# Kernel tuning notes

Hardware: AMD Instinct MI355X
Metric: run time of the kernel (lower is better)

## Reference

```python
import jax, jax.numpy as jnp
import numpy as np

N_LOC = 20000
N_EXP = 200000
H = 64
E = 1500000
L = 400000


def setup_inputs() -> dict:
    key = jax.random.key(0)
    ks = jax.random.split(key, 24)
    f = jnp.float32
    w = lambda k, shp: jax.random.normal(k, shp, dtype=f) * 0.1
    # edges: ('location','of','experts'): src in [0,N_LOC), dst in [0,N_EXP)
    src = jax.random.randint(ks[0], (E,), 0, N_LOC)
    dst = jax.random.randint(ks[1], (E,), 0, N_EXP)
    edge_of = jnp.stack([src, dst])          # location -> experts
    edge_rev = jnp.stack([dst, src])         # experts -> location (ToUndirected)
    row = jax.random.randint(ks[2], (L,), 0, N_LOC)
    col = jax.random.randint(ks[3], (L,), 0, N_EXP)
    edge_label_index = jnp.stack([row, col])
    return dict(
        emb_loc=w(ks[4], (N_LOC, H)), emb_exp=w(ks[5], (N_EXP, H)),
        W1l_of=w(ks[6], (H, H)), b1_of=jnp.zeros((H,), f), W1r_of=w(ks[7], (H, H)),
        W1l_rev=w(ks[8], (H, H)), b1_rev=jnp.zeros((H,), f), W1r_rev=w(ks[9], (H, H)),
        W2l_of=w(ks[10], (H, H)), b2_of=jnp.zeros((H,), f), W2r_of=w(ks[11], (H, H)),
        W2l_rev=w(ks[12], (H, H)), b2_rev=jnp.zeros((H,), f), W2r_rev=w(ks[13], (H, H)),
        dW1=w(ks[14], (2 * H, H)), db1=jnp.zeros((H,), f),
        dW2=w(ks[15], (H, 1)), db2=jnp.zeros((1,), f),
        edge_of=edge_of, edge_rev=edge_rev, edge_label_index=edge_label_index,
    )


def _sage(x_src, x_dst, edge, Wl, b, Wr, n_dst):
    # PyG SAGEConv: lin_l(mean of neighbor msgs) + lin_r(x_dst); bias only in lin_l
    s, d = edge[0], edge[1]
    msg = x_src[s]                                   # [E, H] gather
    summed = jax.ops.segment_sum(msg, d, num_segments=n_dst)
    cnt = jax.ops.segment_sum(jnp.ones((edge.shape[1],), x_src.dtype), d, num_segments=n_dst)
    agg = summed / jnp.maximum(cnt, 1.0)[:, None]
    return agg @ Wl + b + x_dst @ Wr


def reference(emb_loc, emb_exp,
              W1l_of, b1_of, W1r_of, W1l_rev, b1_rev, W1r_rev,
              W2l_of, b2_of, W2r_of, W2l_rev, b2_rev, W2r_rev,
              dW1, db1, dW2, db2,
              edge_of, edge_rev, edge_label_index):
    # layer 1 (to_hetero: one conv per edge type; each dst type has one incoming type)
    z_exp = jax.nn.relu(_sage(emb_loc, emb_exp, edge_of, W1l_of, b1_of, W1r_of, N_EXP))
    z_loc = jax.nn.relu(_sage(emb_exp, emb_loc, edge_rev, W1l_rev, b1_rev, W1r_rev, N_LOC))
    # layer 2 (no relu)
    z_exp2 = _sage(z_loc, z_exp, edge_of, W2l_of, b2_of, W2r_of, N_EXP)
    z_loc2 = _sage(z_exp, z_loc, edge_rev, W2l_rev, b2_rev, W2r_rev, N_LOC)
    # EdgeDecoder: gather-concat-MLP
    row, col = edge_label_index[0], edge_label_index[1]
    z = jnp.concatenate([z_loc2[row], z_exp2[col]], axis=-1)  # [L, 2H]
    h = jax.nn.relu(z @ dW1 + db1)
    out = (h @ dW2 + db2).reshape(-1)
    return out
```

## Files before the change

### kernel.cpp

```cpp
#include <hip/hip_runtime.h>

#define H 64
#define NE 1500000
#define NLOC 20000
#define NEXP 200000
#define NL 400000
#define PAD_E 32
#define PAD_L 128

#define EB 896
#define NBE 224
#define LB 112
#define NBL 179
#define BIN_CHUNK 2048
#define NBIN ((NE + BIN_CHUNK - 1) / BIN_CHUNK)
#define EBSLOT 28
#define LBSLOT 32
#define ECAP 8192
#define LCAP 10240
#define FCAP 4096

#define WS_NEED 90546112ULL

typedef int vint4 __attribute__((ext_vector_type(4)));
typedef _Float16 f16x8 __attribute__((ext_vector_type(8)));
typedef float f32x4 __attribute__((ext_vector_type(4)));
typedef unsigned int u32;
typedef unsigned short u16;
typedef unsigned long long u64;

__device__ __forceinline__ float bcastf(float v, int k) {
  return __int_as_float(__builtin_amdgcn_readlane(__float_as_int(v), k));
}
__device__ __forceinline__ int bcasti(int v, int k) {
  return __builtin_amdgcn_readlane(v, k);
}

__global__ __launch_bounds__(256) void bin_kernel(
    const int* __restrict__ src, const int* __restrict__ dst,
    u32* __restrict__ expQ, u32* __restrict__ locQ,
    int* __restrict__ qcnt, int* __restrict__ flbk_cnt,
    u64* __restrict__ flbkQ)
{
  __shared__ u32 eb[NBE * EBSLOT];
  __shared__ u32 lb[NBL * LBSLOT];
  __shared__ int ec[NBE], lc[NBL], ebase[NBE], lbase[NBL];

  const int tid = threadIdx.x;
  for (int i = tid; i < NBE; i += 256) ec[i] = 0;
  for (int i = tid; i < NBL; i += 256) lc[i] = 0;
  __syncthreads();

  const long base = (long)blockIdx.x * BIN_CHUNK + tid * 8;
  if (base < NE) {
    vint4 s0 = __builtin_nontemporal_load((const vint4*)(src + base));
    vint4 s1 = __builtin_nontemporal_load((const vint4*)(src + base + 4));
    vint4 d0 = __builtin_nontemporal_load((const vint4*)(dst + base));
    vint4 d1 = __builtin_nontemporal_load((const vint4*)(dst + base + 4));
    int ss[8] = {s0.x, s0.y, s0.z, s0.w, s1.x, s1.y, s1.z, s1.w};
    int dd[8] = {d0.x, d0.y, d0.z, d0.w, d1.x, d1.y, d1.z, d1.w};
#pragma unroll
    for (int k = 0; k < 8; k++) {
      const u32 d = (u32)dd[k], s = (u32)ss[k];
      {
        const u32 b = d / (u32)EB;
        const int pos = atomicAdd(&ec[b], 1);
        if (pos < EBSLOT) {
          eb[b * EBSLOT + pos] = ((d - b * EB) << 16) | s;
        } else {
          int fi = atomicAdd(flbk_cnt, 1);
          if (fi < FCAP) flbkQ[fi] = ((u64)d << 32) | (u64)s;
        }
      }
      {
        const u32 b = s / (u32)LB;
        const int pos = atomicAdd(&lc[b], 1);
        if (pos < LBSLOT) {
          lb[b * LBSLOT + pos] = ((s - b * LB) << 18) | d;
        } else {
          int fi = atomicAdd(flbk_cnt, 1);
          if (fi < FCAP) flbkQ[fi] = (1ULL << 63) | ((u64)s << 32) | (u64)d;
        }
      }
    }
  }
  __syncthreads();

  for (int i = tid; i < NBE; i += 256) {
    const int c = min(ec[i], EBSLOT);
    ebase[i] = c ? atomicAdd(&qcnt[i], c) : 0;
  }
  for (int i = tid; i < NBL; i += 256) {
    const int c = min(lc[i], LBSLOT);
    lbase[i] = c ? atomicAdd(&qcnt[NBE + i], c) : 0;
  }
  __syncthreads();

  const int wid = tid >> 6, ln = tid & 63;
  for (int b = wid; b < NBE; b += 4) {
    const int c = min(ec[b], EBSLOT);
    if (ln < c) {
      const int idx = ebase[b] + ln;
      const u32 r = eb[b * EBSLOT + ln];
      if (idx < ECAP) {
        expQ[(long)b * ECAP + idx] = r;
      } else {
        int fi = atomicAdd(flbk_cnt, 1);
        if (fi < FCAP)
          flbkQ[fi] = ((u64)(b * EB + (r >> 16)) << 32) | (u64)(r & 0xFFFF);
      }
    }
  }
  for (int b = wid; b < NBL; b += 4) {
    const int c = min(lc[b], LBSLOT);
    if (ln < c) {
      const int idx = lbase[b] + ln;
      const u32 r = lb[b * LBSLOT + ln];
      if (idx < LCAP) {
        locQ[(long)b * LCAP + idx] = r;
      } else {
        int fi = atomicAdd(flbk_cnt, 1);
        if (fi < FCAP)
          flbkQ[fi] = (1ULL << 63) | ((u64)(b * LB + (r >> 18)) << 32) |
                      (u64)(r & 0x3FFFF);
      }
    }
  }
}

__global__ __launch_bounds__(256) void build_kernel(
    const u32* __restrict__ expQ, const u32* __restrict__ locQ,
    const int* __restrict__ qcnt,
    u16* __restrict__ nbr_exp, int* __restrict__ nbr_loc,
    int* __restrict__ cnt_exp, int* __restrict__ cnt_loc)
{
  __shared__ char ldsraw[60928];
  const int tid = threadIdx.x;
  if (blockIdx.x < NBE) {
    const int b = blockIdx.x;
    u16* rows = (u16*)ldsraw;
    int* cnts = (int*)(ldsraw + 57344);
    for (int i = tid; i < EB; i += 256) cnts[i] = 0;
    __syncthreads();
    const int n = min(qcnt[b], ECAP);
    for (int i = tid; i < n; i += 256) {
      const u32 r = expQ[(long)b * ECAP + i];
      const int nl = (int)(r >> 16);
      const int pos = atomicAdd(&cnts[nl], 1);
      if (pos < PAD_E) rows[nl * PAD_E + pos] = (u16)(r & 0xFFFF);
    }
    __syncthreads();
    const int node0 = b * EB;
    const int nn = min(EB, NEXP - node0);
    u32* grows = (u32*)(nbr_exp + (long)node0 * PAD_E);
    const u32* lrows = (const u32*)rows;
    for (int j = tid; j < nn * (PAD_E / 2); j += 256) grows[j] = lrows[j];
    for (int i = tid; i < nn; i += 256) cnt_exp[node0 + i] = cnts[i];
  } else {
    const int b = blockIdx.x - NBE;
    int* rows = (int*)ldsraw;
    int* cnts = (int*)(ldsraw + 57344);
    for (int i = tid; i < LB; i += 256) cnts[i] = 0;
    __syncthreads();
    const int n = min(qcnt[NBE + b], LCAP);
    for (int i = tid; i < n; i += 256) {
      const u32 r = locQ[(long)b * LCAP + i];
      const int sl = (int)(r >> 18);
      const int pos = atomicAdd(&cnts[sl], 1);
      if (pos < PAD_L) rows[sl * PAD_L + pos] = (int)(r & 0x3FFFF);
    }
    __syncthreads();
    const int node0 = b * LB;
    const int nn = min(LB, NLOC - node0);
    int* grows = nbr_loc + (long)node0 * PAD_L;
    for (int j = tid; j < nn * PAD_L; j += 256) grows[j] = rows[j];
    for (int i = tid; i < nn; i += 256) cnt_loc[node0 + i] = cnts[i];
  }
}

__global__ __launch_bounds__(256) void fold_kernel(
    const float* __restrict__ W2r_of, const float* __restrict__ W2l_of,
    const float* __restrict__ W2l_rev, const float* __restrict__ W2r_rev,
    const float* __restrict__ dW1, const float* __restrict__ b2_of,
    const float* __restrict__ b2_rev,
    float* __restrict__ Wf_q, float* __restrict__ Wf_y2,
    float* __restrict__ Wf_t2, float* __restrict__ Wf_p,
    float* __restrict__ bf_q, float* __restrict__ bf_p,
    const int* __restrict__ flbk_cnt, const u64* __restrict__ flbkQ,
    u16* __restrict__ nbr_exp, int* __restrict__ nbr_loc,
    int* __restrict__ cnt_exp, int* __restrict__ cnt_loc)
{
  const int lane = threadIdx.x & 63;
  const int w = threadIdx.x >> 6;
  const float* dW1a = dW1;
  const float* dW1b = dW1 + H * H;
  if (blockIdx.x < 4) {
    const float* A; const float* B; float* C;
    switch (blockIdx.x) {
      case 0:  A = W2r_of;  B = dW1b; C = Wf_q;  break;
      case 1:  A = W2l_of;  B = dW1b; C = Wf_y2; break;
      case 2:  A = W2l_rev; B = dW1a; C = Wf_t2; break;
      default: A = W2r_rev; B = dW1a; C = Wf_p;  break;
    }
    float b[H];
#pragma unroll
    for (int k = 0; k < H; k++) b[k] = B[k * H + lane];
    for (int r = w * 16; r < w * 16 + 16; r++) {
      const float xv = A[r * H + lane];
      float a0 = 0.f, a1 = 0.f;
#pragma unroll
      for (int k = 0; k < H; k += 2) {
        a0 += bcastf(xv, k)     * b[k];
        a1 += bcastf(xv, k + 1) * b[k + 1];
      }
      C[r * H + lane] = a0 + a1;
    }
  } else if (blockIdx.x == 4) {
    if (w < 2) {
      const float* bv_src = (w == 0) ? b2_of : b2_rev;
      const float* B      = (w == 0) ? dW1b  : dW1a;
      float* o            = (w == 0) ? bf_q  : bf_p;
      float wk[H];
#pragma unroll
      for (int k = 0; k < H; k++) wk[k] = B[k * H + lane];
      const float bv = bv_src[lane];
      float a = 0.f;
#pragma unroll
      for (int k = 0; k < H; k++) a += bcastf(bv, k) * wk[k];
      o[lane] = a;
    }
  } else {
    const int n = min(*flbk_cnt, FCAP);
    for (int i = threadIdx.x; i < n; i += 256) {
      const u64 rec = flbkQ[i];
      const int node = (int)((rec >> 32) & 0x3FFFF);
      const int val  = (int)(rec & 0x3FFFF);
      if ((rec >> 63) == 0) {
        int pos = atomicAdd(&cnt_exp[node], 1);
        if (pos < PAD_E) nbr_exp[(long)node * PAD_E + pos] = (u16)val;
      } else {
        int pos = atomicAdd(&cnt_loc[node], 1);
        if (pos < PAD_L) nbr_loc[(long)node * PAD_L + pos] = val;
      }
    }
  }
}

__global__ __launch_bounds__(256, 4) void dense_linear_kernel(
    const float* __restrict__ x, _Float16* __restrict__ out16,
    const float* __restrict__ W, int n)
{
  const int lane = threadIdx.x & 63;
  const int gw = (blockIdx.x * 256 + threadIdx.x) >> 6;
  const int nw = (gridDim.x * 256) >> 6;
  float w[H];
#pragma unroll
  for (int k = 0; k < H; k++) w[k] = W[k * H + lane];
  for (int i = gw; i < n; i += nw) {
    const float xv = x[i * H + lane];
    float a0 = 0.f, a1 = 0.f;
#pragma unroll
    for (int k = 0; k < H; k += 2) {
      a0 += bcastf(xv, k)     * w[k];
      a1 += bcastf(xv, k + 1) * w[k + 1];
    }
    out16[i * H + lane] = (_Float16)(a0 + a1);
  }
}

__global__ __launch_bounds__(256, 4) void mfma_pass_kernel(
    const unsigned short* __restrict__ nbr, const int* __restrict__ cnt,
    const _Float16* __restrict__ y,
    const float* a32, const _Float16* a16,
    _Float16* out1, const float* __restrict__ W1,
    const float* __restrict__ bias, int relu,
    _Float16* out2, const float* __restrict__ W2)
{
  const int w = threadIdx.x >> 6;
  const int lane = threadIdx.x & 63;
  const int q = lane >> 4;
  const int cidx = lane & 15;
  const int rb = blockIdx.x * 16;

  __shared__ float Gs[16 * H];

  f16x8 b1lo, b1hi, b2lo, b2hi;
#pragma unroll
  for (int j = 0; j < 8; j++) {
    b1lo[j] = (_Float16)W1[(q * 8 + j) * H + w * 16 + cidx];
    b1hi[j] = (_Float16)W1[(32 + q * 8 + j) * H + w * 16 + cidx];
  }
  if (out2) {
#pragma unroll
    for (int j = 0; j < 8; j++) {
      b2lo[j] = (_Float16)W2[(q * 8 + j) * H + w * 16 + cidx];
      b2hi[j] = (_Float16)W2[(32 + q * 8 + j) * H + w * 16 + cidx];
    }
  }

  if (y) {
    for (int rr = 0; rr < 4; rr++) {
      const int i = rb + w * 4 + rr;
      const int c = cnt[i];
      const int cc = min(c, PAD_E);
      const unsigned short* nb = nbr + (long)i * PAD_E;
      float s0 = 0.f, s1 = 0.f, s2 = 0.f, s3 = 0.f;
      const int id = (lane < cc) ? (int)nb[lane] : 0;
      int k = 0;
      const int m4 = cc & ~3;
      for (; k < m4; k += 4) {
        const int i0 = bcasti(id, k), i1 = bcasti(id, k + 1),
                  i2 = bcasti(id, k + 2), i3 = bcasti(id, k + 3);
        s0 += (float)y[(long)i0 * H + lane];
        s1 += (float)y[(long)i1 * H + lane];
        s2 += (float)y[(long)i2 * H + lane];
        s3 += (float)y[(long)i3 * H + lane];
      }
      for (; k < cc; k++) s0 += (float)y[(long)bcasti(id, k) * H + lane];
      Gs[(w * 4 + rr) * H + lane] =
          ((s0 + s1) + (s2 + s3)) / fmaxf((float)c, 1.0f);
    }
  }

  f16x8 a0, a1;
  if (a16) {
    const _Float16* ar = a16 + (long)(rb + cidx) * H;
    a0 = *(const f16x8*)(ar + q * 8);
    a1 = *(const f16x8*)(ar + 32 + q * 8);
  } else {
    const float* ar = a32 + (long)(rb + cidx) * H;
#pragma unroll
    for (int j = 0; j < 8; j++) {
      a0[j] = (_Float16)ar[q * 8 + j];
      a1[j] = (_Float16)ar[32 + q * 8 + j];
    }
  }
  f32x4 acc1 = {0.f, 0.f, 0.f, 0.f};
  acc1 = __builtin_amdgcn_mfma_f32_16x16x32_f16(a0, b1lo, acc1, 0, 0, 0);
  acc1 = __builtin_amdgcn_mfma_f32_16x16x32_f16(a1, b1hi, acc1, 0, 0, 0);
  f32x4 acc2 = {0.f, 0.f, 0.f, 0.f};
  if (out2) {
    acc2 = __builtin_amdgcn_mfma_f32_16x16x32_f16(a0, b2lo, acc2, 0, 0, 0);
    acc2 = __builtin_amdgcn_mfma_f32_16x16x32_f16(a1, b2hi, acc2, 0, 0, 0);
  }

  const float bj = bias ? bias[w * 16 + cidx] : 0.f;
  __syncthreads();
#pragma unroll
  for (int reg = 0; reg < 4; reg++) {
    const int r = q * 4 + reg;
    float v = acc1[reg] + bj;
    if (y) v += Gs[r * H + w * 16 + cidx];
    if (relu) v = fmaxf(v, 0.f);
    out1[(long)(rb + r) * H + w * 16 + cidx] = (_Float16)v;
    if (out2)
      out2[(long)(rb + r) * H + w * 16 + cidx] = (_Float16)acc2[reg];
  }
}

__global__ __launch_bounds__(256, 4) void loc_gather_kernel(
    const int* __restrict__ nbr, const int* __restrict__ cnt,
    const _Float16* __restrict__ T, const float* __restrict__ x,
    float* __restrict__ out32, _Float16* __restrict__ out16,
    const float* __restrict__ Wr, const float* __restrict__ bias,
    int n, int relu)
{
  const int lane = threadIdx.x & 63;
  const int gw = (blockIdx.x * 256 + threadIdx.x) >> 6;
  const int nw = (gridDim.x * 256) >> 6;
  float wr[H];
#pragma unroll
  for (int k = 0; k < H; k++) wr[k] = Wr[k * H + lane];
  const float bj = bias[lane];
  for (int i = gw; i < n; i += nw) {
    const int c = cnt[i];
    const int cc = min(c, PAD_L);
    const int* nb = nbr + (long)i * PAD_L;
    float s0 = 0.f, s1 = 0.f, s2 = 0.f, s3 = 0.f;
    int e = 0;
    while (e < cc) {
      const int m = min(cc - e, 64);
      const int id = (lane < m) ? nb[e + lane] : 0;
      int k = 0;
      const int m4 = m & ~3;
      for (; k < m4; k += 4) {
        const int i0 = bcasti(id, k), i1 = bcasti(id, k + 1),
                  i2 = bcasti(id, k + 2), i3 = bcasti(id, k + 3);
        s0 += (float)T[(long)i0 * H + lane];
        s1 += (float)T[(long)i1 * H + lane];
        s2 += (float)T[(long)i2 * H + lane];
        s3 += (float)T[(long)i3 * H + lane];
      }
      for (; k < m; k++) s0 += (float)T[(long)bcasti(id, k) * H + lane];
      e += m;
    }
    const float agg = ((s0 + s1) + (s2 + s3)) / fmaxf((float)c, 1.0f);
    const float xv = x[i * H + lane];
    float a0 = 0.f, a1 = 0.f;
#pragma unroll
    for (int k = 0; k < H; k += 2) {
      a0 += bcastf(xv, k)     * wr[k];
      a1 += bcastf(xv, k + 1) * wr[k + 1];
    }
    float acc = agg + bj + a0 + a1;
    if (relu) acc = fmaxf(acc, 0.0f);
    if (out32) out32[i * H + lane] = acc;
    else       out16[i * H + lane] = (_Float16)acc;
  }
}

__global__ __launch_bounds__(256, 4) void edge_kernel(
    const int* __restrict__ row, const int* __restrict__ col,
    const _Float16* __restrict__ P, const _Float16* __restrict__ Q,
    const float* __restrict__ db1, const float* __restrict__ dW2,
    const float* __restrict__ db2, float* __restrict__ out)
{
  const int lane = threadIdx.x & 63;
  const int gw = (blockIdx.x * 256 + threadIdx.x) >> 6;
  const int nw = (gridDim.x * 256) >> 6;
  const float bj = db1[lane];
  const float w2 = dW2[lane];
  const float b2 = db2[0];
  for (int e = gw * 4; e < NL; e += nw * 4) {
    const int n4 = min(NL - e, 4);
    float h[4];
#pragma unroll
    for (int k = 0; k < 4; k++) {
      if (k < n4) {
        const int r = row[e + k], c = col[e + k];
        const float p = (float)P[(long)r * H + lane];
        const float q = (float)Q[(long)c * H + lane];
        h[k] = fmaxf(p + q + bj, 0.0f) * w2;
      } else h[k] = 0.f;
    }
#pragma unroll
    for (int off = 1; off < 64; off <<= 1) {
#pragma unroll
      for (int k = 0; k < 4; k++) h[k] += __shfl_xor(h[k], off);
    }
    if (lane == 0) {
#pragma unroll
      for (int k = 0; k < 4; k++)
        if (k < n4) out[e + k] = h[k] + b2;
    }
  }
}

extern "C" void kernel_launch(void* const* d_in, const int* in_sizes, int n_in,
                              void* d_out, int out_size, void* d_ws, size_t ws_size,
                              hipStream_t stream) {
  const float* emb_loc = (const float*)d_in[0];
  const float* emb_exp = (const float*)d_in[1];
  const float* W1l_of  = (const float*)d_in[2];
  const float* b1_of   = (const float*)d_in[3];
  const float* W1r_of  = (const float*)d_in[4];
  const float* W1l_rev = (const float*)d_in[5];
  const float* b1_rev  = (const float*)d_in[6];
  const float* W1r_rev = (const float*)d_in[7];
  const float* W2l_of  = (const float*)d_in[8];
  const float* b2_of   = (const float*)d_in[9];
  const float* W2r_of  = (const float*)d_in[10];
  const float* W2l_rev = (const float*)d_in[11];
  const float* b2_rev  = (const float*)d_in[12];
  const float* W2r_rev = (const float*)d_in[13];
  const float* dW1     = (const float*)d_in[14];
  const float* db1     = (const float*)d_in[15];
  const float* dW2     = (const float*)d_in[16];
  const float* db2     = (const float*)d_in[17];
  const int*   edge_of = (const int*)d_in[18];
  const int*   eli     = (const int*)d_in[20];

  const int* src = edge_of;
  const int* dst = edge_of + NE;
  const int* row = eli;
  const int* col = eli + NL;

  if (ws_size < WS_NEED) return;

  char* ws = (char*)d_ws;
  int*            cnt_loc = (int*)(ws);
  int*            cnt_exp = (int*)(ws + 80000);
  int*            nbr_loc = (int*)(ws + 880064);
  unsigned short* nbr_exp = (unsigned short*)(ws + 11120064);
  _Float16*       Ylh     = (_Float16*)(ws + 23920064);
  _Float16*       Y2fh    = (_Float16*)(ws + 26480064);
  float*          z_loc   = (float*)(ws + 29040064);
  _Float16*       PH      = (_Float16*)(ws + 34160064);
  _Float16*       ZE      = (_Float16*)(ws + 39280064);
  _Float16*       TH      = (_Float16*)(ws + 64880064);
  u32*            expQ    = (u32*)(ws + 64880064);
  u32*            locQ    = (u32*)(ws + 72220096);
  int*            qcnt    = (int*)(ws + 79551936);
  int*            flbk    = (int*)(ws + 79553552);
  u64*            flbkQ   = (u64*)(ws + 79554048);
  float*          Wf_q    = (float*)(ws + 90480064);
  float*          Wf_y2   = (float*)(ws + 90496448);
  float*          Wf_t2   = (float*)(ws + 90512832);
  float*          Wf_p    = (float*)(ws + 90529216);
  float*          bf_q    = (float*)(ws + 90545600);
  float*          bf_p    = (float*)(ws + 90545856);
  float*          out     = (float*)d_out;

  (void)hipMemsetAsync(ws + 79551936, 0, 2048, stream);

  bin_kernel<<<NBIN, 256, 0, stream>>>(src, dst, expQ, locQ, qcnt, flbk, flbkQ);
  build_kernel<<<NBE + NBL, 256, 0, stream>>>(expQ, locQ, qcnt,
      nbr_exp, nbr_loc, cnt_exp, cnt_loc);
  fold_kernel<<<6, 256, 0, stream>>>(W2r_of, W2l_of, W2l_rev, W2r_rev,
                                     dW1, b2_of, b2_rev,
                                     Wf_q, Wf_y2, Wf_t2, Wf_p, bf_q, bf_p,
                                     flbk, flbkQ, nbr_exp, nbr_loc,
                                     cnt_exp, cnt_loc);

  dense_linear_kernel<<<1280, 256, 0, stream>>>(emb_loc, Ylh, W1l_of, NLOC);
  mfma_pass_kernel<<<NEXP / 16, 256, 0, stream>>>(nbr_exp, cnt_exp, Ylh,
      emb_exp, (const _Float16*)nullptr, ZE, W1r_of, b1_of, 1, TH, W1l_rev);
  loc_gather_kernel<<<1250, 256, 0, stream>>>(nbr_loc, cnt_loc, TH,
      emb_loc, z_loc, (_Float16*)nullptr, W1r_rev, b1_rev, NLOC, 1);

  dense_linear_kernel<<<1280, 256, 0, stream>>>(z_loc, Y2fh, Wf_y2, NLOC);
  mfma_pass_kernel<<<NEXP / 16, 256, 0, stream>>>(nbr_exp, cnt_exp, Y2fh,
      (const float*)nullptr, ZE, ZE, Wf_q, bf_q, 0, TH, Wf_t2);
  loc_gather_kernel<<<1250, 256, 0, stream>>>(nbr_loc, cnt_loc, TH,
      z_loc, (float*)nullptr, PH, Wf_p, bf_p, NLOC, 0);

  edge_kernel<<<2048, 256, 0, stream>>>(row, col, PH, ZE,
                                        db1, dW2, db2, out);
}
```

Measured before the change: 527.1 us.

## Fuse first dense linear into prep kernel and interleave neighbor gathers for ILP

Merges the layer-1 location dense linear (emb_loc @ W1l_of) into the weight-folding prep kernel, which saves one launch. In mfma_pass the A-operand loads are vectorized and moved ahead of the neighbor gather. The gather now loops over four rows at once so more independent loads are in flight, and the shared buffer is padded to 68 floats per row. loc_gather now handles two nodes per wave with interleaved gathers. The cost is more branchy predicated loops, and the dense linear now runs on only 314 blocks instead of 1280.

```diff
diff --git a/kernel.cpp b/kernel.cpp
--- a/kernel.cpp
+++ b/kernel.cpp
@@ -178,7 +178,7 @@
   }
 }
 
-__global__ __launch_bounds__(256) void fold_kernel(
+__global__ __launch_bounds__(256) void prep_kernel(
     const float* __restrict__ W2r_of, const float* __restrict__ W2l_of,
     const float* __restrict__ W2l_rev, const float* __restrict__ W2r_rev,
     const float* __restrict__ dW1, const float* __restrict__ b2_of,
@@ -188,7 +188,9 @@
     float* __restrict__ bf_q, float* __restrict__ bf_p,
     const int* __restrict__ flbk_cnt, const u64* __restrict__ flbkQ,
     u16* __restrict__ nbr_exp, int* __restrict__ nbr_loc,
-    int* __restrict__ cnt_exp, int* __restrict__ cnt_loc)
+    int* __restrict__ cnt_exp, int* __restrict__ cnt_loc,
+    const float* __restrict__ emb_loc, _Float16* __restrict__ Ylh,
+    const float* __restrict__ W1l_of)
 {
   const int lane = threadIdx.x & 63;
   const int w = threadIdx.x >> 6;
@@ -229,7 +231,7 @@
       for (int k = 0; k < H; k++) a += bcastf(bv, k) * wk[k];
       o[lane] = a;
     }
-  } else {
+  } else if (blockIdx.x == 5) {
     const int n = min(*flbk_cnt, FCAP);
     for (int i = threadIdx.x; i < n; i += 256) {
       const u64 rec = flbkQ[i];
@@ -243,6 +245,23 @@
         if (pos < PAD_L) nbr_loc[(long)node * PAD_L + pos] = val;
       }
     }
+  } else {
+    float wreg[H];
+#pragma unroll
+    for (int k = 0; k < H; k++) wreg[k] = W1l_of[k * H + lane];
+    const int rbase = (blockIdx.x - 6) * 64 + w * 16;
+    for (int rr = 0; rr < 16; rr++) {
+      const int r = rbase + rr;
+      if (r >= NLOC) break;
+      const float xv = emb_loc[(long)r * H + lane];
+      float a0 = 0.f, a1 = 0.f;
+#pragma unroll
+      for (int k = 0; k < H; k += 2) {
+        a0 += bcastf(xv, k)     * wreg[k];
+        a1 += bcastf(xv, k + 1) * wreg[k + 1];
+      }
+      Ylh[(long)r * H + lane] = (_Float16)(a0 + a1);
+    }
   }
 }
 
@@ -269,7 +288,7 @@
 }
 
 __global__ __launch_bounds__(256, 4) void mfma_pass_kernel(
-    const unsigned short* __restrict__ nbr, const int* __restrict__ cnt,
+    const u16* __restrict__ nbr, const int* __restrict__ cnt,
     const _Float16* __restrict__ y,
     const float* a32, const _Float16* a16,
     _Float16* out1, const float* __restrict__ W1,
@@ -282,7 +301,7 @@
   const int cidx = lane & 15;
   const int rb = blockIdx.x * 16;
 
-  __shared__ float Gs[16 * H];
+  __shared__ float Gs[16 * 68];
 
   f16x8 b1lo, b1hi, b2lo, b2hi;
 #pragma unroll
@@ -295,30 +314,6 @@
     for (int j = 0; j < 8; j++) {
       b2lo[j] = (_Float16)W2[(q * 8 + j) * H + w * 16 + cidx];
       b2hi[j] = (_Float16)W2[(32 + q * 8 + j) * H + w * 16 + cidx];
-    }
-  }
-
-  if (y) {
-    for (int rr = 0; rr < 4; rr++) {
-      const int i = rb + w * 4 + rr;
-      const int c = cnt[i];
-      const int cc = min(c, PAD_E);
-      const unsigned short* nb = nbr + (long)i * PAD_E;
-      float s0 = 0.f, s1 = 0.f, s2 = 0.f, s3 = 0.f;
-      const int id = (lane < cc) ? (int)nb[lane] : 0;
-      int k = 0;
-      const int m4 = cc & ~3;
-      for (; k < m4; k += 4) {
-        const int i0 = bcasti(id, k), i1 = bcasti(id, k + 1),
-                  i2 = bcasti(id, k + 2), i3 = bcasti(id, k + 3);
-        s0 += (float)y[(long)i0 * H + lane];
-        s1 += (float)y[(long)i1 * H + lane];
-        s2 += (float)y[(long)i2 * H + lane];
-        s3 += (float)y[(long)i3 * H + lane];
-      }
-      for (; k < cc; k++) s0 += (float)y[(long)bcasti(id, k) * H + lane];
-      Gs[(w * 4 + rr) * H + lane] =
-          ((s0 + s1) + (s2 + s3)) / fmaxf((float)c, 1.0f);
     }
   }
 
@@ -329,12 +324,48 @@
     a1 = *(const f16x8*)(ar + 32 + q * 8);
   } else {
     const float* ar = a32 + (long)(rb + cidx) * H;
-#pragma unroll
-    for (int j = 0; j < 8; j++) {
-      a0[j] = (_Float16)ar[q * 8 + j];
-      a1[j] = (_Float16)ar[32 + q * 8 + j];
-    }
-  }
+    f32x4 v0 = *(const f32x4*)(ar + q * 8);
+    f32x4 v1 = *(const f32x4*)(ar + q * 8 + 4);
+    f32x4 v2 = *(const f32x4*)(ar + 32 + q * 8);
+    f32x4 v3 = *(const f32x4*)(ar + 32 + q * 8 + 4);
+#pragma unroll
+    for (int j = 0; j < 4; j++) {
+      a0[j] = (_Float16)v0[j];
+      a0[j + 4] = (_Float16)v1[j];
+      a1[j] = (_Float16)v2[j];
+      a1[j + 4] = (_Float16)v3[j];
+    }
+  }
+
+  if (y) {
+    const int i0r = rb + w * 4;
+    int c4[4];
+#pragma unroll
+    for (int rr = 0; rr < 4; rr++) c4[rr] = cnt[i0r + rr];
+    int id4[4];
+#pragma unroll
+    for (int rr = 0; rr < 4; rr++) {
+      const int c = min(c4[rr], PAD_E);
+      id4[rr] = (lane < c) ? (int)nbr[(long)(i0r + rr) * PAD_E + lane] : 0;
+    }
+    float sa[4] = {0.f, 0.f, 0.f, 0.f}, sb[4] = {0.f, 0.f, 0.f, 0.f};
+    const int cm = min(max(max(c4[0], c4[1]), max(c4[2], c4[3])), PAD_E);
+    for (int k = 0; k < cm; k += 2) {
+#pragma unroll
+      for (int rr = 0; rr < 4; rr++) {
+        const int c = min(c4[rr], PAD_E);
+        if (k < c)
+          sa[rr] += (float)y[(long)bcasti(id4[rr], k) * H + lane];
+        if (k + 1 < c)
+          sb[rr] += (float)y[(long)bcasti(id4[rr], k + 1) * H + lane];
+      }
+    }
+#pragma unroll
+    for (int rr = 0; rr < 4; rr++)
+      Gs[(w * 4 + rr) * 68 + lane] =
+          (sa[rr] + sb[rr]) / fmaxf((float)c4[rr], 1.0f);
+  }
+
   f32x4 acc1 = {0.f, 0.f, 0.f, 0.f};
   acc1 = __builtin_amdgcn_mfma_f32_16x16x32_f16(a0, b1lo, acc1, 0, 0, 0);
   acc1 = __builtin_amdgcn_mfma_f32_16x16x32_f16(a1, b1hi, acc1, 0, 0, 0);
@@ -350,7 +381,7 @@
   for (int reg = 0; reg < 4; reg++) {
     const int r = q * 4 + reg;
     float v = acc1[reg] + bj;
-    if (y) v += Gs[r * H + w * 16 + cidx];
+    if (y) v += Gs[r * 68 + w * 16 + cidx];
     if (relu) v = fmaxf(v, 0.f);
     out1[(long)(rb + r) * H + w * 16 + cidx] = (_Float16)v;
     if (out2)
@@ -372,40 +403,52 @@
 #pragma unroll
   for (int k = 0; k < H; k++) wr[k] = Wr[k * H + lane];
   const float bj = bias[lane];
-  for (int i = gw; i < n; i += nw) {
-    const int c = cnt[i];
-    const int cc = min(c, PAD_L);
-    const int* nb = nbr + (long)i * PAD_L;
-    float s0 = 0.f, s1 = 0.f, s2 = 0.f, s3 = 0.f;
-    int e = 0;
-    while (e < cc) {
-      const int m = min(cc - e, 64);
-      const int id = (lane < m) ? nb[e + lane] : 0;
-      int k = 0;
-      const int m4 = m & ~3;
-      for (; k < m4; k += 4) {
-        const int i0 = bcasti(id, k), i1 = bcasti(id, k + 1),
-                  i2 = bcasti(id, k + 2), i3 = bcasti(id, k + 3);
-        s0 += (float)T[(long)i0 * H + lane];
-        s1 += (float)T[(long)i1 * H + lane];
-        s2 += (float)T[(long)i2 * H + lane];
-        s3 += (float)T[(long)i3 * H + lane];
-      }
-      for (; k < m; k++) s0 += (float)T[(long)bcasti(id, k) * H + lane];
-      e += m;
-    }
-    const float agg = ((s0 + s1) + (s2 + s3)) / fmaxf((float)c, 1.0f);
-    const float xv = x[i * H + lane];
-    float a0 = 0.f, a1 = 0.f;
+  for (int i = gw * 2; i < n; i += nw * 2) {
+    const int c0 = cnt[i], c1 = cnt[i + 1];
+    const int cc0 = min(c0, PAD_L), cc1 = min(c1, PAD_L);
+    const int* nb0 = nbr + (long)i * PAD_L;
+    const int* nb1 = nb0 + PAD_L;
+    float s0a = 0.f, s0b = 0.f, s1a = 0.f, s1b = 0.f;
+    for (int e = 0; e < PAD_L; e += 64) {
+      const int m0 = min(cc0 - e, 64);
+      const int m1 = min(cc1 - e, 64);
+      if (m0 <= 0 && m1 <= 0) break;
+      const int id0 = (lane < m0) ? nb0[e + lane] : 0;
+      const int id1 = (lane < m1) ? nb1[e + lane] : 0;
+      const int km = max(m0, m1);
+      for (int k = 0; k < km; k += 2) {
+        if (k < m0)
+          s0a += (float)T[(long)bcasti(id0, k) * H + lane];
+        if (k + 1 < m0)
+          s0b += (float)T[(long)bcasti(id0, k + 1) * H + lane];
+        if (k < m1)
+          s1a += (float)T[(long)bcasti(id1, k) * H + lane];
+        if (k + 1 < m1)
+          s1b += (float)T[(long)bcasti(id1, k + 1) * H + lane];
+      }
+    }
+    const float agg0 = (s0a + s0b) / fmaxf((float)c0, 1.0f);
+    const float agg1 = (s1a + s1b) / fmaxf((float)c1, 1.0f);
+    const float xv0 = x[(long)i * H + lane];
+    const float xv1 = x[(long)(i + 1) * H + lane];
+    float a00 = 0.f, a01 = 0.f, a10 = 0.f, a11 = 0.f;
 #pragma unroll
     for (int k = 0; k < H; k += 2) {
-      a0 += bcastf(xv, k)     * wr[k];
-      a1 += bcastf(xv, k + 1) * wr[k + 1];
-    }
-    float acc = agg + bj + a0 + a1;
-    if (relu) acc = fmaxf(acc, 0.0f);
-    if (out32) out32[i * H + lane] = acc;
-    else       out16[i * H + lane] = (_Float16)acc;
+      a00 += bcastf(xv0, k)     * wr[k];
+      a01 += bcastf(xv0, k + 1) * wr[k + 1];
+      a10 += bcastf(xv1, k)     * wr[k];
+      a11 += bcastf(xv1, k + 1) * wr[k + 1];
+    }
+    float acc0 = agg0 + bj + a00 + a01;
+    float acc1 = agg1 + bj + a10 + a11;
+    if (relu) { acc0 = fmaxf(acc0, 0.0f); acc1 = fmaxf(acc1, 0.0f); }
+    if (out32) {
+      out32[(long)i * H + lane] = acc0;
+      out32[(long)(i + 1) * H + lane] = acc1;
+    } else {
+      out16[(long)i * H + lane] = (_Float16)acc0;
+      out16[(long)(i + 1) * H + lane] = (_Float16)acc1;
+    }
   }
 }
 
@@ -506,13 +549,13 @@
   bin_kernel<<<NBIN, 256, 0, stream>>>(src, dst, expQ, locQ, qcnt, flbk, flbkQ);
   build_kernel<<<NBE + NBL, 256, 0, stream>>>(expQ, locQ, qcnt,
       nbr_exp, nbr_loc, cnt_exp, cnt_loc);
-  fold_kernel<<<6, 256, 0, stream>>>(W2r_of, W2l_of, W2l_rev, W2r_rev,
-                                     dW1, b2_of, b2_rev,
-                                     Wf_q, Wf_y2, Wf_t2, Wf_p, bf_q, bf_p,
-                                     flbk, flbkQ, nbr_exp, nbr_loc,
-                                     cnt_exp, cnt_loc);
-
-  dense_linear_kernel<<<1280, 256, 0, stream>>>(emb_loc, Ylh, W1l_of, NLOC);
+  prep_kernel<<<320, 256, 0, stream>>>(W2r_of, W2l_of, W2l_rev, W2r_rev,
+                                       dW1, b2_of, b2_rev,
+                                       Wf_q, Wf_y2, Wf_t2, Wf_p, bf_q, bf_p,
+                                       flbk, flbkQ, nbr_exp, nbr_loc,
+                                       cnt_exp, cnt_loc,
+                                       emb_loc, Ylh, W1l_of);
+
   mfma_pass_kernel<<<NEXP / 16, 256, 0, stream>>>(nbr_exp, cnt_exp, Ylh,
       emb_exp, (const _Float16*)nullptr, ZE, W1r_of, b1_of, 1, TH, W1l_rev);
   loc_gather_kernel<<<1250, 256, 0, stream>>>(nbr_loc, cnt_loc, TH,
```

Result: slower. 703.4 us (+33.4%).
